# Kernel tuning notes

Hardware: AMD Instinct MI355X
Metric: run time of the kernel (lower is better)

## Reference

```python
import jax, jax.numpy as jnp
import numpy as np

N_QUBITS = 10
Q_DEPTH = 6


def _apply_1q(state, gate, wire):
    """Apply a 2x2 gate (or batched [B,2,2] gates) to `wire` of state [B,2,...,2]."""
    s = jnp.moveaxis(state, wire + 1, -1)
    if gate.ndim == 2:
        s = s @ gate.T  # new_j = sum_i G[j,i] * old_i
    else:
        s = jnp.einsum('b...i,bji->b...j', s, gate)
    return jnp.moveaxis(s, -1, wire + 1)


def _apply_cnot(state, ctrl, tgt):
    s = jnp.moveaxis(state, (ctrl + 1, tgt + 1), (-2, -1))
    s = jnp.stack([s[..., 0, :], s[..., 1, ::-1]], axis=-2)  # flip target where ctrl=1
    return jnp.moveaxis(s, (-2, -1), (ctrl + 1, tgt + 1))


def _ry(theta):
    """RY(theta) = [[cos(t/2), -sin(t/2)], [sin(t/2), cos(t/2)]]; theta scalar or [B]."""
    c, s = jnp.cos(theta / 2.0), jnp.sin(theta / 2.0)
    return jnp.stack([jnp.stack([c, -s], -1), jnp.stack([s, c], -1)], -2)


def _vqc(angles, q_weights):
    """angles: [B, n_qubits] per-sample RY angles; q_weights: [q_depth, n_qubits].
    Returns <PauliZ_w> for every wire: [B, n_qubits]. All gates are real -> float32 state."""
    B, n = angles.shape
    q_depth = q_weights.shape[0]
    # H-layer on |0...0> gives the uniform superposition: all amplitudes 2^{-n/2}
    state = jnp.full((B,) + (2,) * n, 2.0 ** (-n / 2.0), dtype=angles.dtype)
    # RY layer with per-sample input angles
    for w in range(n):
        state = _apply_1q(state, _ry(angles[:, w]), w)
    # q_depth x (brick-wall CNOT entangler + trainable RY layer)
    for k in range(q_depth):
        for i in range(0, n - 1, 2):
            state = _apply_cnot(state, i, i + 1)
        for i in range(1, n - 1, 2):
            state = _apply_cnot(state, i, i + 1)
        for w in range(n):
            state = _apply_1q(state, _ry(q_weights[k, w]), w)
    # expval(PauliZ(w)) = P(wire w = 0) - P(wire w = 1)
    probs = state * state  # real statevector
    exps = []
    for w in range(n):
        p = jnp.moveaxis(probs, w + 1, 1).reshape(B, 2, -1).sum(-1)
        exps.append(p[:, 0] - p[:, 1])
    return jnp.stack(exps, -1)


def setup_inputs() -> dict:
    key = jax.random.key(0)
    ks = jax.random.split(key, 6)
    B, D_IN, OUT = 8192, 512, 64
    x = jax.random.normal(ks[0], (B, D_IN), dtype=jnp.float32)
    W1 = jax.random.normal(ks[1], (D_IN, N_QUBITS), dtype=jnp.float32) * (1.0 / np.sqrt(D_IN))
    b1 = jnp.zeros((N_QUBITS,), dtype=jnp.float32)
    # keras 'uniform' initializer: U(-0.05, 0.05)
    q_weights = jax.random.uniform(ks[2], (Q_DEPTH, N_QUBITS), dtype=jnp.float32,
                                   minval=-0.05, maxval=0.05)
    W2 = jax.random.normal(ks[3], (N_QUBITS, OUT), dtype=jnp.float32) * (1.0 / np.sqrt(N_QUBITS))
    b2 = jnp.zeros((OUT,), dtype=jnp.float32)
    return {"x": x, "W1": W1, "b1": b1, "q_weights": q_weights, "W2": W2, "b2": b2}


def reference(x, W1, b1, q_weights, W2, b2):
    # Dense(n_qubits, tanh) then scale to angles in (-pi/2, pi/2)
    angles = jnp.tanh(x @ W1 + b1) * (jnp.pi / 2.0)  # [B, n_qubits]
    q_out = _vqc(angles, q_weights)                   # [B, n_qubits]
    return q_out @ W2 + b2                            # [B, output_dim]
```

## Files before the change

kernel.cpp:

```cpp
#include <hip/hip_runtime.h>

#define NQ 10
#define QD 6
#define DIN 512
#define DOUT 64

template <int CTRL>
__device__ __forceinline__ float dppf(float v) {
    return __int_as_float(__builtin_amdgcn_mov_dpp(__float_as_int(v), CTRL, 0xF, 0xF, true));
}
template <int M>
__device__ __forceinline__ float sx(float v) {
    if constexpr (M == 1)       return dppf<0xB1>(v);
    else if constexpr (M == 2)  return dppf<0x4E>(v);
    else if constexpr (M == 4)  return dppf<0x1B>(dppf<0x141>(v));
    else                        return dppf<0x128>(v);
}
__device__ __forceinline__ float swz16(float v) {
    return __int_as_float(__builtin_amdgcn_ds_swizzle(__float_as_int(v), 0x401F));
}
__device__ __forceinline__ float sx32(float v, int xaddr) {
    return __int_as_float(__builtin_amdgcn_ds_bpermute(xaddr, __float_as_int(v)));
}
__device__ __forceinline__ float red64(float v, int xaddr) {
    v += dppf<0x128>(v); v += dppf<0x124>(v);
    v += dppf<0x122>(v); v += dppf<0x121>(v);
    v += swz16(v);
    v += sx32(v, xaddr);
    return v;
}
__device__ __forceinline__ float tanh_fast(float x) {
    const float e = __expf(2.0f * x);
    return 1.0f - __fdividef(2.0f, e + 1.0f);
}

__global__ __launch_bounds__(256) void dqc_main(
    const float* __restrict__ x,
    const float* __restrict__ W1,
    const float* __restrict__ b1,
    const float* __restrict__ qw,
    const float* __restrict__ W2,
    const float* __restrict__ b2,
    float* __restrict__ out,
    const int B)
{
    __shared__ __align__(16) float csl[QD * 24];
    __shared__ __align__(16) float tsl[QD * 8];

    const int tid = threadIdx.x;
    if (tid < QD * NQ) {
        const int layer = tid / NQ, wire = tid - layer * NQ;
        const float h = qw[tid] * 0.5f;
        const float s = __sinf(h), c = __cosf(h);
        const int pos = layer * 24 + (wire & 1) * 12 + (wire >> 1) * 2;
        csl[pos] = c; csl[pos + 1] = s;
        int slot = -1;
        if (wire == 0) slot = 0; else if (wire == 7) slot = 1;
        else if (wire == 8) slot = 2; else if (wire == 9) slot = 3;
        else if (wire == 1) slot = 4; else if (wire == 3) slot = 5;
        else if (wire == 5) slot = 6;
        if (slot >= 0) tsl[layer * 8 + slot] = __fdividef(s, c);
    }

    const int lane = tid & 63;
    const int b = blockIdx.x * 4 + (tid >> 6);
    const int bb = (b < B) ? b : (B - 1);
    const int xaddr = ((tid ^ 32) & 63) << 2;

    float xr[8];
    {
        const float4* xp = (const float4*)(x + (size_t)bb * DIN + lane * 8);
        const float4 v0 = xp[0], v1 = xp[1];
        xr[0]=v0.x; xr[1]=v0.y; xr[2]=v0.z; xr[3]=v0.w;
        xr[4]=v1.x; xr[5]=v1.y; xr[6]=v1.z; xr[7]=v1.w;
    }
    float dot[NQ];
    #pragma unroll
    for (int w = 0; w < NQ; ++w) dot[w] = 0.f;
    {
        const float4* wp = (const float4*)(W1 + (size_t)lane * 8 * NQ);
        #pragma unroll
        for (int j = 0; j < 4; ++j) {
            const float4 f0 = wp[5*j], f1 = wp[5*j+1], f2 = wp[5*j+2],
                         f3 = wp[5*j+3], f4 = wp[5*j+4];
            const float xa = xr[2*j], xb = xr[2*j+1];
            dot[0]=fmaf(xa,f0.x,dot[0]); dot[1]=fmaf(xa,f0.y,dot[1]);
            dot[2]=fmaf(xa,f0.z,dot[2]); dot[3]=fmaf(xa,f0.w,dot[3]);
            dot[4]=fmaf(xa,f1.x,dot[4]); dot[5]=fmaf(xa,f1.y,dot[5]);
            dot[6]=fmaf(xa,f1.z,dot[6]); dot[7]=fmaf(xa,f1.w,dot[7]);
            dot[8]=fmaf(xa,f2.x,dot[8]); dot[9]=fmaf(xa,f2.y,dot[9]);
            dot[0]=fmaf(xb,f2.z,dot[0]); dot[1]=fmaf(xb,f2.w,dot[1]);
            dot[2]=fmaf(xb,f3.x,dot[2]); dot[3]=fmaf(xb,f3.y,dot[3]);
            dot[4]=fmaf(xb,f3.z,dot[4]); dot[5]=fmaf(xb,f3.w,dot[5]);
            dot[6]=fmaf(xb,f4.x,dot[6]); dot[7]=fmaf(xb,f4.y,dot[7]);
            dot[8]=fmaf(xb,f4.z,dot[8]); dot[9]=fmaf(xb,f4.w,dot[9]);
        }
    }
    #pragma unroll
    for (int w = 0; w < NQ; ++w) dot[w] = red64(dot[w], xaddr);

    float u0[NQ], u1[NQ];
    #pragma unroll
    for (int w = 0; w < NQ; ++w) {
        const float phi = fmaf(tanh_fast(dot[w] + b1[w]),
                               0.78539816339744830962f, 0.78539816339744830962f);
        u0[w] = __cosf(phi);
        u1[w] = __sinf(phi);
    }

    __syncthreads();

    float F = 1.f;
    #pragma unroll
    for (int k = 0; k < QD; ++k) {
        const float* ce = csl + k * 24;
        F *= ce[0] * ce[18];
        F *= ce[8] * ce[20];
    }
    {   const float* c5 = csl + 5 * 24;
        F *= c5[12] * c5[14];
        F *= c5[16];
    }

    float A[16];
    {
        float lf = ((lane & 32) ? u1[0] : u0[0]);
        lf *= ((((lane >> 4) ^ (lane >> 5)) & 1) ? u1[1] : u0[1]);
        lf *= ((lane & 8) ? u1[2] : u0[2]);
        lf *= ((((lane >> 2) ^ (lane >> 3)) & 1) ? u1[3] : u0[3]);
        lf *= ((lane & 2) ? u1[4] : u0[4]);
        lf *= (((lane ^ (lane >> 1)) & 1) ? u1[5] : u0[5]);
        lf *= F;
        float d1[2] = { lf * u0[6], lf * u1[6] };
        float d2[4], d3[8];
        #pragma unroll
        for (int i = 0; i < 4; ++i) {
            const int r3 = i >> 1, r2 = i & 1;
            d2[i] = d1[r3] * (((r2 ^ r3) & 1) ? u1[7] : u0[7]);
        }
        #pragma unroll
        for (int i = 0; i < 8; ++i)
            d3[i] = d2[i >> 1] * ((i & 1) ? u1[8] : u0[8]);
        #pragma unroll
        for (int i = 0; i < 8; ++i) {
            const int r1 = i & 1;
            A[2*i]   = d3[i] * (r1 ? u1[9] : u0[9]);
            A[2*i+1] = d3[i] * (r1 ? u0[9] : u1[9]);
        }
    }

    #pragma unroll 1
    for (int k = 0; k < QD; ++k) {
        const float* ce = csl + k * 24;
        const float4 ea = *(const float4*)(ce);
        const float4 eb = *(const float4*)(ce + 4);
        const float4 tv = *(const float4*)(tsl + k * 8);
        const float C2=ea.z,S2=ea.w, C4=eb.x,S4=eb.y, C6=eb.z,S6=eb.w;
        const float T0=tv.x, T7=tv.y, T8=tv.z, T9=tv.w;

        {
            const float t0 = (lane & 32) ? T0 : -T0;
            float p[16];
            #pragma unroll
            for (int r = 0; r < 16; ++r) p[r] = sx32(A[r], xaddr);
            #pragma unroll
            for (int r = 0; r < 16; ++r) A[r] = fmaf(t0, p[r], A[r]);
        }
        {
            const float g = (lane & 8) ? S2 : -S2;
            const bool cb = (lane & 16) != 0;
            const float al = cb ? g : C2, be = cb ? C2 : g;
            #pragma unroll
            for (int r = 0; r < 16; ++r) A[r] = fmaf(al, A[r], be * sx<8>(A[r]));
        }
        {
            const float g = (lane & 2) ? S4 : -S4;
            const bool cb = (lane & 4) != 0;
            const float al = cb ? g : C4, be = cb ? C4 : g;
            #pragma unroll
            for (int r = 0; r < 16; ++r) A[r] = fmaf(al, A[r], be * sx<2>(A[r]));
        }
        {
            const bool cb = (lane & 1) != 0;
            const float a_lo = cb ? -S6 : C6, b_lo = cb ? C6 : -S6;
            const float a_hi = cb ?  S6 : C6, b_hi = cb ? C6 :  S6;
            #pragma unroll
            for (int r = 0; r < 8; ++r) {
                const float lo = A[r], hi = A[r + 8];
                A[r]     = fmaf(a_lo, lo, b_lo * hi);
                A[r + 8] = fmaf(a_hi, hi, b_hi * lo);
            }
        }
        {
            #pragma unroll
            for (int r = 0; r < 16; ++r) {
                if (r & 2) continue;
                const float lo = A[r], hi = A[r + 2];
                if (r & 4) {
                    A[r]     = fmaf(-T8, lo, hi);
                    A[r + 2] = fmaf( T8, hi, lo);
                } else {
                    A[r]     = fmaf(-T8, hi, lo);
                    A[r + 2] = fmaf( T8, lo, hi);
                }
            }
        }

        if (k != QD - 1) {
            const float4 oa = *(const float4*)(ce + 12);
            const float2 ob = *(const float2*)(ce + 16);
            const float C1=oa.x,S1=oa.y, C3=oa.z,S3=oa.w, C5=ob.x,S5=ob.y;

            {
                const float g = (lane & 16) ? S1 : -S1;
                const bool cb = (lane & 32) != 0;
                const float al = cb ? -g : C1, be = cb ? C1 : g;
                float p[16];
                #pragma unroll
                for (int r = 0; r < 16; ++r) p[r] = swz16(A[r]);
                #pragma unroll
                for (int r = 0; r < 16; ++r) A[r] = fmaf(al, A[r], be * p[r]);
            }
            {
                const float g = (lane & 4) ? S3 : -S3;
                const bool cb = (lane & 8) != 0;
                const float al = cb ? -g : C3, be = cb ? C3 : g;
                #pragma unroll
                for (int r = 0; r < 16; ++r) A[r] = fmaf(al, A[r], be * sx<4>(A[r]));
            }
            {
                const float g = (lane & 1) ? S5 : -S5;
                const bool cb = (lane & 2) != 0;
                const float al = cb ? -g : C5, be = cb ? C5 : g;
                #pragma unroll
                for (int r = 0; r < 16; ++r) A[r] = fmaf(al, A[r], be * sx<1>(A[r]));
            }
            {
                #pragma unroll
                for (int r = 0; r < 16; ++r) {
                    if (r & 4) continue;
                    const float lo = A[r], hi = A[r + 4];
                    if (r & 8) {
                        A[r]     = fmaf( T7, lo, hi);
                        A[r + 4] = fmaf(-T7, hi, lo);
                    } else {
                        A[r]     = fmaf(-T7, hi, lo);
                        A[r + 4] = fmaf( T7, lo, hi);
                    }
                }
            }
            {
                #pragma unroll
                for (int r = 0; r < 16; r += 2) {
                    const float xv = A[r], yv = A[r + 1];
                    if (r & 2) {
                        A[r]     = fmaf( T9, xv, yv);
                        A[r + 1] = fmaf(-T9, yv, xv);
                    } else {
                        A[r]     = fmaf(-T9, yv, xv);
                        A[r + 1] = fmaf( T9, xv, yv);
                    }
                }
            }
        } else {
            const float4 tv2 = *(const float4*)(tsl + k * 8 + 4);
            const float T1 = tv2.x, T3 = tv2.y, T5 = tv2.z;

            {
                const float t1 = (lane & 16) ? T1 : -T1;
                float p[16];
                #pragma unroll
                for (int r = 0; r < 16; ++r) p[r] = swz16(A[r]);
                #pragma unroll
                for (int r = 0; r < 16; ++r) A[r] = fmaf(t1, p[r], A[r]);
            }
            {
                const float t3 = (lane & 4) ? T3 : -T3;
                #pragma unroll
                for (int r = 0; r < 16; ++r) A[r] = fmaf(t3, sx<4>(A[r]), A[r]);
            }
            {
                const float t5 = (lane & 1) ? T5 : -T5;
                #pragma unroll
                for (int r = 0; r < 16; ++r) A[r] = fmaf(t5, sx<1>(A[r]), A[r]);
            }
            {
                #pragma unroll
                for (int r = 0; r < 16; ++r) {
                    if (r & 4) continue;
                    const float lo = A[r], hi = A[r + 4];
                    A[r]     = fmaf(-T7, hi, lo);
                    A[r + 4] = fmaf( T7, lo, hi);
                }
            }
            {
                #pragma unroll
                for (int r = 0; r < 16; r += 2) {
                    const float xv = A[r], yv = A[r + 1];
                    A[r]     = fmaf(-T9, yv, xv);
                    A[r + 1] = fmaf( T9, xv, yv);
                }
            }
        }
    }

    float tot = 0.f, q6 = 0.f, q7 = 0.f, q8 = 0.f, q9 = 0.f;
    #pragma unroll
    for (int r = 0; r < 16; ++r) {
        const float P = A[r] * A[r];
        tot += P;
        if (r & 8) q6 += P;
        if (r & 4) q7 += P;
        if (r & 2) q8 += P;
        if (r & 1) q9 += P;
    }
    float e[NQ];
    e[0] = (lane & 32) ? -tot : tot;
    e[1] = (lane & 16) ? -tot : tot;
    e[2] = (lane & 8)  ? -tot : tot;
    e[3] = (lane & 4)  ? -tot : tot;
    e[4] = (lane & 2)  ? -tot : tot;
    e[5] = (lane & 1)  ? -tot : tot;
    e[6] = fmaf(-2.f, q6, tot);
    e[7] = fmaf(-2.f, q7, tot);
    e[8] = fmaf(-2.f, q8, tot);
    e[9] = fmaf(-2.f, q9, tot);
    #pragma unroll
    for (int w = 0; w < NQ; ++w) e[w] = red64(e[w], xaddr);

    if (b < B) {
        float o = b2[lane];
        #pragma unroll
        for (int w = 0; w < NQ; ++w) o = fmaf(e[w], W2[w * DOUT + lane], o);
        out[(size_t)b * DOUT + lane] = o;
    }
}

extern "C" void kernel_launch(void* const* d_in, const int* in_sizes, int n_in,
                              void* d_out, int out_size, void* d_ws, size_t ws_size,
                              hipStream_t stream) {
    const float* x  = (const float*)d_in[0];
    const float* W1 = (const float*)d_in[1];
    const float* b1 = (const float*)d_in[2];
    const float* qw = (const float*)d_in[3];
    const float* W2 = (const float*)d_in[4];
    const float* b2 = (const float*)d_in[5];
    float* out = (float*)d_out;

    const int B = in_sizes[0] / DIN;
    const int blocks = (B + 3) / 4;
    dqc_main<<<blocks, 256, 0, stream>>>(x, W1, b1, qw, W2, b2, out, B);
}
```

Measured before the change: 99.50 us.

## Replace LDS-based cross-row lane exchanges with permlane16/32 swap instructions

Swaps the ds_bpermute and ds_swizzle cross-half and cross-row lane exchanges in the qubit gate loop and in the reductions for v_permlane32_swap and v_permlane16_swap, which are VALU register swaps. Because these swap pairs of registers, gates on wires 0 and 1 are now applied register-pair-wise through a swap, compute, swap-back pattern, and wire 1 is rewritten in tangent form with its cosine folded into the global factor F. The final reductions combine several values per swap (fin4/fin2) to cut the number of exchanges. A fallback path keeps LDS permutes where the builtins are unavailable, and the extra swap-back instructions add VALU work.

```diff
diff --git a/kernel.cpp b/kernel.cpp
--- a/kernel.cpp
+++ b/kernel.cpp
@@ -16,19 +16,77 @@
     else if constexpr (M == 4)  return dppf<0x1B>(dppf<0x141>(v));
     else                        return dppf<0x128>(v);
 }
-__device__ __forceinline__ float swz16(float v) {
-    return __int_as_float(__builtin_amdgcn_ds_swizzle(__float_as_int(v), 0x401F));
-}
-__device__ __forceinline__ float sx32(float v, int xaddr) {
-    return __int_as_float(__builtin_amdgcn_ds_bpermute(xaddr, __float_as_int(v)));
-}
-__device__ __forceinline__ float red64(float v, int xaddr) {
+
+#if __has_builtin(__builtin_amdgcn_permlane32_swap)
+__device__ __forceinline__ void pl32(float& a, float& b) {
+    auto r = __builtin_amdgcn_permlane32_swap(__float_as_int(a), __float_as_int(b), false, false);
+    a = __int_as_float(r[0]); b = __int_as_float(r[1]);
+}
+#else
+__device__ __forceinline__ void pl32(float& a, float& b) {
+    const int lane = threadIdx.x & 63;
+    const int xaddr = ((threadIdx.x ^ 32) & 63) << 2;
+    const float pa = __int_as_float(__builtin_amdgcn_ds_bpermute(xaddr, __float_as_int(a)));
+    const float pb = __int_as_float(__builtin_amdgcn_ds_bpermute(xaddr, __float_as_int(b)));
+    const bool hi = (lane & 32) != 0;
+    const float na = hi ? pb : a;
+    const float nb = hi ? b  : pa;
+    a = na; b = nb;
+}
+#endif
+#if __has_builtin(__builtin_amdgcn_permlane16_swap)
+__device__ __forceinline__ void pl16(float& a, float& b) {
+    auto r = __builtin_amdgcn_permlane16_swap(__float_as_int(a), __float_as_int(b), false, false);
+    a = __int_as_float(r[0]); b = __int_as_float(r[1]);
+}
+#else
+__device__ __forceinline__ void pl16(float& a, float& b) {
+    const int lane = threadIdx.x & 63;
+    const float pa = __int_as_float(__builtin_amdgcn_ds_swizzle(__float_as_int(a), 0x401F));
+    const float pb = __int_as_float(__builtin_amdgcn_ds_swizzle(__float_as_int(b), 0x401F));
+    const bool odd = (lane & 16) != 0;
+    const float na = odd ? pb : a;
+    const float nb = odd ? b  : pa;
+    a = na; b = nb;
+}
+#endif
+
+__device__ __forceinline__ void gate_pl32(float& u, float& v, float T) {
+    pl32(u, v);
+    float n0 = fmaf(-T, v, u);
+    float n1 = fmaf( T, u, v);
+    pl32(n0, n1);
+    u = n0; v = n1;
+}
+__device__ __forceinline__ void gate_pl16(float& u, float& v, float T, bool cswap) {
+    pl16(u, v);
+    const float q0 = fmaf(-T, v, u);
+    const float q1 = fmaf( T, u, v);
+    float n0 = cswap ? q1 : q0;
+    float n1 = cswap ? q0 : q1;
+    pl16(n0, n1);
+    u = n0; v = n1;
+}
+
+__device__ __forceinline__ float rowred(float v) {
     v += dppf<0x128>(v); v += dppf<0x124>(v);
     v += dppf<0x122>(v); v += dppf<0x121>(v);
-    v += swz16(v);
-    v += sx32(v, xaddr);
     return v;
 }
+__device__ __forceinline__ void fin4(float& a, float& b, float& c, float& d) {
+    pl16(a, b); float z0 = a + b;
+    pl16(c, d); float z1 = c + d;
+    pl32(z0, z1); float t = z0 + z1;
+    float u = t; pl32(t, u);
+    b = t; pl16(t, b); a = t;
+    d = u; pl16(u, d); c = u;
+}
+__device__ __forceinline__ void fin2(float& a, float& b) {
+    pl16(a, b); float z = a + b;
+    float z2 = z; pl32(z, z2); float t = z + z2;
+    b = t; pl16(t, b); a = t;
+}
+
 __device__ __forceinline__ float tanh_fast(float x) {
     const float e = __expf(2.0f * x);
     return 1.0f - __fdividef(2.0f, e + 1.0f);
@@ -65,7 +123,6 @@
     const int lane = tid & 63;
     const int b = blockIdx.x * 4 + (tid >> 6);
     const int bb = (b < B) ? b : (B - 1);
-    const int xaddr = ((tid ^ 32) & 63) << 2;
 
     float xr[8];
     {
@@ -97,7 +154,10 @@
         }
     }
     #pragma unroll
-    for (int w = 0; w < NQ; ++w) dot[w] = red64(dot[w], xaddr);
+    for (int w = 0; w < NQ; ++w) dot[w] = rowred(dot[w]);
+    fin4(dot[0], dot[1], dot[2], dot[3]);
+    fin4(dot[4], dot[5], dot[6], dot[7]);
+    fin2(dot[8], dot[9]);
 
     float u0[NQ], u1[NQ];
     #pragma unroll
@@ -116,10 +176,10 @@
         const float* ce = csl + k * 24;
         F *= ce[0] * ce[18];
         F *= ce[8] * ce[20];
+        F *= ce[12];
     }
     {   const float* c5 = csl + 5 * 24;
-        F *= c5[12] * c5[14];
-        F *= c5[16];
+        F *= c5[14] * c5[16];
     }
 
     float A[16];
@@ -155,16 +215,15 @@
         const float4 ea = *(const float4*)(ce);
         const float4 eb = *(const float4*)(ce + 4);
         const float4 tv = *(const float4*)(tsl + k * 8);
+        const float4 tw = *(const float4*)(tsl + k * 8 + 4);
         const float C2=ea.z,S2=ea.w, C4=eb.x,S4=eb.y, C6=eb.z,S6=eb.w;
         const float T0=tv.x, T7=tv.y, T8=tv.z, T9=tv.w;
+        const float T1=tw.x;
 
         {
-            const float t0 = (lane & 32) ? T0 : -T0;
-            float p[16];
             #pragma unroll
-            for (int r = 0; r < 16; ++r) p[r] = sx32(A[r], xaddr);
-            #pragma unroll
-            for (int r = 0; r < 16; ++r) A[r] = fmaf(t0, p[r], A[r]);
+            for (int i = 0; i < 8; ++i)
+                gate_pl32(A[2*i], A[2*i+1], T0);
         }
         {
             const float g = (lane & 8) ? S2 : -S2;
@@ -209,17 +268,13 @@
         if (k != QD - 1) {
             const float4 oa = *(const float4*)(ce + 12);
             const float2 ob = *(const float2*)(ce + 16);
-            const float C1=oa.x,S1=oa.y, C3=oa.z,S3=oa.w, C5=ob.x,S5=ob.y;
-
-            {
-                const float g = (lane & 16) ? S1 : -S1;
+            const float C3=oa.z,S3=oa.w, C5=ob.x,S5=ob.y;
+
+            {
                 const bool cb = (lane & 32) != 0;
-                const float al = cb ? -g : C1, be = cb ? C1 : g;
-                float p[16];
-                #pragma unroll
-                for (int r = 0; r < 16; ++r) p[r] = swz16(A[r]);
-                #pragma unroll
-                for (int r = 0; r < 16; ++r) A[r] = fmaf(al, A[r], be * p[r]);
+                #pragma unroll
+                for (int i = 0; i < 8; ++i)
+                    gate_pl16(A[2*i], A[2*i+1], T1, cb);
             }
             {
                 const float g = (lane & 4) ? S3 : -S3;
@@ -263,16 +318,12 @@
                 }
             }
         } else {
-            const float4 tv2 = *(const float4*)(tsl + k * 8 + 4);
-            const float T1 = tv2.x, T3 = tv2.y, T5 = tv2.z;
-
-            {
-                const float t1 = (lane & 16) ? T1 : -T1;
-                float p[16];
-                #pragma unroll
-                for (int r = 0; r < 16; ++r) p[r] = swz16(A[r]);
-                #pragma unroll
-                for (int r = 0; r < 16; ++r) A[r] = fmaf(t1, p[r], A[r]);
+            const float T3 = tw.y, T5 = tw.z;
+
+            {
+                #pragma unroll
+                for (int i = 0; i < 8; ++i)
+                    gate_pl16(A[2*i], A[2*i+1], T1, false);
             }
             {
                 const float t3 = (lane & 4) ? T3 : -T3;
@@ -326,7 +377,10 @@
     e[8] = fmaf(-2.f, q8, tot);
     e[9] = fmaf(-2.f, q9, tot);
     #pragma unroll
-    for (int w = 0; w < NQ; ++w) e[w] = red64(e[w], xaddr);
+    for (int w = 0; w < NQ; ++w) e[w] = rowred(e[w]);
+    fin4(e[0], e[1], e[2], e[3]);
+    fin4(e[4], e[5], e[6], e[7]);
+    fin2(e[8], e[9]);
 
     if (b < B) {
         float o = b2[lane];
```

Measured after the change: 106.3 us. +6.8%, slower.
